# Optimization experiments

Hardware: AMD Instinct MI355X
Metric: run time of the kernel (lower is better)

The kernel has to match this reference:

```python
import jax, jax.numpy as jnp
import numpy as np

EPS = 1e-6
ALPHA = 0.2  # LeakyReLU negative slope


def layer_norm(x, g, b):
    mu = jnp.mean(x, axis=-1, keepdims=True)
    var = jnp.mean(jnp.square(x - mu), axis=-1, keepdims=True)
    return (x - mu) * jax.lax.rsqrt(var + EPS) * g + b


def graph_attention(x, bias, W, a_src, a_dst):
    # x: [B,N,D], bias: [B,N,N], W: [D, H*Dh], a_src/a_dst: [H, Dh]
    B, N, D = x.shape
    H, Dh = a_src.shape
    h = jnp.einsum('bnd,dhk->bhnk', x, W.reshape(D, H, Dh))  # [B,H,N,Dh]
    s = jnp.einsum('bhnk,hk->bhn', h, a_src)                 # source term
    t = jnp.einsum('bhnk,hk->bhn', h, a_dst)                 # target term
    e = jax.nn.leaky_relu(s[:, :, :, None] + t[:, :, None, :], ALPHA)
    e = e + bias[:, None, :, :]                              # graph mask/bias
    attn = jax.nn.softmax(e, axis=-1)                        # [B,H,N,N]
    out = jnp.einsum('bhij,bhjk->bhik', attn, h)             # [B,H,N,Dh]
    return out.transpose(0, 2, 1, 3).reshape(B, N, H * Dh)


def setup_inputs() -> dict:
    key = jax.random.key(0)
    ks = jax.random.split(key, 8)
    B, N, D, H = 2, 2048, 512, 8
    Dh = D // H
    sc = 1.0 / np.sqrt(D)
    return {
        'x': jax.random.normal(ks[0], (B, N, D), jnp.float32),
        'bias': jax.random.normal(ks[1], (B, N, N), jnp.float32),
        'W1': jax.random.normal(ks[2], (D, D), jnp.float32) * sc,
        'a_src1': jax.random.normal(ks[3], (H, Dh), jnp.float32) * sc,
        'a_dst1': jax.random.normal(ks[4], (H, Dh), jnp.float32) * sc,
        'g1': jnp.ones((D,), jnp.float32),
        'b1': jnp.zeros((D,), jnp.float32),
        'W2': jax.random.normal(ks[5], (D, D), jnp.float32) * sc,
        'a_src2': jax.random.normal(ks[6], (1, D), jnp.float32) * sc,
        'a_dst2': jax.random.normal(ks[7], (1, D), jnp.float32) * sc,
        'g2': jnp.ones((D,), jnp.float32),
        'b2': jnp.zeros((D,), jnp.float32),
    }


def reference(x, bias, W1, a_src1, a_dst1, g1, b1, W2, a_src2, a_dst2, g2, b2):
    # dropout is identity in eval mode
    attn_in = layer_norm(x, g1, b1)
    attn = graph_attention(attn_in, bias, W1, a_src1, a_dst1) + x
    attn_in2 = layer_norm(attn, g2, b2)
    out = graph_attention(attn_in2, bias, W2, a_src2, a_dst2) + attn
    return out
```

## Files before the change

kernel.cpp:

```cpp
#include <hip/hip_runtime.h>
#include <math.h>

#define NB 2
#define NN 2048
#define DD 512
#define L2E 1.44269504088896340736f

typedef __attribute__((ext_vector_type(8))) short short8;
typedef __attribute__((ext_vector_type(4))) float f32x4;

__device__ __forceinline__ unsigned short f2bf(float x) {
  union { float f; unsigned u; } a;
  a.f = x;
  unsigned r = a.u + 0x7FFF + ((a.u >> 16) & 1);
  return (unsigned short)(r >> 16);
}
__device__ __forceinline__ float bf2f(unsigned short u) {
  union { unsigned u; float f; } a;
  a.u = ((unsigned)u) << 16;
  return a.f;
}
__device__ __forceinline__ unsigned cvtpk(float lo, float hi) {
  unsigned r;
  asm("v_cvt_pk_bf16_f32 %0, %1, %2" : "=v"(r) : "v"(lo), "v"(hi));
  return r;
}
__device__ __forceinline__ uint2 exp4pk(float e0, float e1, float e2, float e3) {
  float p0, p1, p2, p3;
  uint2 d;
  asm("v_exp_f32 %2, %6\n\t"
      "v_exp_f32 %3, %7\n\t"
      "v_exp_f32 %4, %8\n\t"
      "v_exp_f32 %5, %9\n\t"
      "v_cvt_pk_bf16_f32 %0, %2, %3\n\t"
      "v_cvt_pk_bf16_f32 %1, %4, %5"
      : "=&v"(d.x), "=&v"(d.y), "=&v"(p0), "=&v"(p1), "=&v"(p2), "=&v"(p3)
      : "v"(e0), "v"(e1), "v"(e2), "v"(e3));
  return d;
}

__device__ __forceinline__ float waveReduceSum(float v) {
#pragma unroll
  for (int o = 32; o; o >>= 1) v += __shfl_down(v, o, 64);
  return v;
}
__device__ __forceinline__ float blockReduceSum(float v, float* red4) {
  int tid = threadIdx.x;
  __syncthreads();
  v = waveReduceSum(v);
  if ((tid & 63) == 0) red4[tid >> 6] = v;
  __syncthreads();
  return red4[0] + red4[1] + red4[2] + red4[3];
}

__global__ __launch_bounds__(256) void prep_kernel(
    const float* __restrict__ W1, const float* __restrict__ W2,
    unsigned short* __restrict__ WT1, unsigned short* __restrict__ WT2,
    const float* __restrict__ as1, const float* __restrict__ ad1,
    float* __restrict__ vs1, float* __restrict__ vd1,
    const float* __restrict__ as2, const float* __restrict__ ad2,
    float* __restrict__ vs2, float* __restrict__ vd2) {
  __shared__ float tile[64][65];
  int bid = blockIdx.x;
  int t = threadIdx.x;
  if (bid < 128) {
    const float* W = (bid & 64) ? W2 : W1;
    unsigned short* WT = (bid & 64) ? WT2 : WT1;
    int r = bid & 63;
    int kt = (r >> 3) * 64, ct = (r & 7) * 64;
#pragma unroll
    for (int u = 0; u < 16; u++) {
      int lin = t + u * 256;
      int kl = lin >> 6, cl = lin & 63;
      tile[kl][cl] = W[(size_t)(kt + kl) * DD + ct + cl];
    }
    __syncthreads();
#pragma unroll
    for (int u = 0; u < 16; u++) {
      int lin = t + u * 256;
      int cl = lin >> 6, kl = lin & 63;
      WT[(size_t)(ct + cl) * DD + kt + kl] = f2bf(tile[kl][cl]);
    }
  } else {
    int idx = bid - 128;
    int slot = idx >> 3, dch = idx & 7;
    const float *W, *as, *ad;
    float *vs, *vd;
    int Dh, hoff;
    if (slot < 8) {
      W = W1; as = as1 + slot * 64; ad = ad1 + slot * 64;
      vs = vs1 + (size_t)slot * DD; vd = vd1 + (size_t)slot * DD;
      Dh = 64; hoff = slot * 64;
    } else {
      W = W2; as = as2; ad = ad2; vs = vs2; vd = vd2;
      Dh = 512; hoff = 0;
    }
    int dl = t >> 2, kq = t & 3;
    int d = dch * 64 + dl;
    int kn = Dh >> 2;
    const float* wr = W + (size_t)d * DD + hoff + kq * kn;
    const float* asp = as + kq * kn;
    const float* adp = ad + kq * kn;
    float s = 0.f, dd2 = 0.f;
    for (int k = 0; k < kn; k++) {
      float wv = wr[k];
      s += wv * asp[k];
      dd2 += wv * adp[k];
    }
    s += __shfl_xor(s, 1);
    s += __shfl_xor(s, 2);
    dd2 += __shfl_xor(dd2, 1);
    dd2 += __shfl_xor(dd2, 2);
    if (kq == 0) {
      vs[d] = s;
      vd[d] = dd2;
    }
  }
}

__global__ __launch_bounds__(256) void lnst_kernel(
    const float* __restrict__ x, const float* __restrict__ g,
    const float* __restrict__ bb, unsigned short* __restrict__ y,
    const float* __restrict__ vs, const float* __restrict__ vd,
    float* __restrict__ sOut, float* __restrict__ tOut, int HN) {
  __shared__ float red4[4];
  __shared__ float lnS[512];
  int row = blockIdx.x;
  int t = threadIdx.x;
  const float* xr = x + (size_t)row * DD;
  float2 v = *(const float2*)&xr[2 * t];
  float s = blockReduceSum(v.x + v.y, red4);
  float mu = s * (1.0f / 512.0f);
  float d0 = v.x - mu, d1 = v.y - mu;
  float ss = blockReduceSum(d0 * d0 + d1 * d1, red4);
  float rstd = rsqrtf(ss * (1.0f / 512.0f) + 1e-6f);
  float2 gg = *(const float2*)&g[2 * t];
  float2 bv = *(const float2*)&bb[2 * t];
  float n0 = d0 * rstd * gg.x + bv.x;
  float n1 = d1 * rstd * gg.y + bv.y;
  ushort2 o;
  o.x = f2bf(n0);
  o.y = f2bf(n1);
  *(ushort2*)&y[(size_t)row * DD + 2 * t] = o;
  lnS[2 * t] = n0;
  lnS[2 * t + 1] = n1;
  __syncthreads();
  int wv = t >> 6, l = t & 63;
  int b = row >> 11, n = row & (NN - 1);
  float4 x0 = *(const float4*)&lnS[l * 8];
  float4 x1 = *(const float4*)&lnS[l * 8 + 4];
  for (int h = wv; h < HN; h += 4) {
    const float* vsr = vs + (size_t)h * DD + l * 8;
    const float* vdr = vd + (size_t)h * DD + l * 8;
    float4 a0 = *(const float4*)vsr, a1 = *(const float4*)(vsr + 4);
    float4 c0 = *(const float4*)vdr, c1 = *(const float4*)(vdr + 4);
    float ps = x0.x * a0.x + x0.y * a0.y + x0.z * a0.z + x0.w * a0.w +
               x1.x * a1.x + x1.y * a1.y + x1.z * a1.z + x1.w * a1.w;
    float pd = x0.x * c0.x + x0.y * c0.y + x0.z * c0.z + x0.w * c0.w +
               x1.x * c1.x + x1.y * c1.y + x1.z * c1.z + x1.w * c1.w;
#pragma unroll
    for (int o2 = 32; o2; o2 >>= 1) {
      ps += __shfl_xor(ps, o2);
      pd += __shfl_xor(pd, o2);
    }
    if (l == 0) {
      sOut[((size_t)b * HN + h) * NN + n] = ps * L2E;
      tOut[((size_t)b * HN + h) * NN + n] = pd * L2E;
    }
  }
}

__global__ __launch_bounds__(256) void gemm_kernel(const unsigned short* __restrict__ A,
                                                   const unsigned short* __restrict__ BT,
                                                   unsigned short* __restrict__ hbT) {
  __shared__ float accL[4][16][65];
  int t = threadIdx.x, w = t >> 6, l = t & 63;
  int li = l & 15, lg = l >> 4;
  int R0 = blockIdx.x * 16;
  int c0 = blockIdx.y * 64;
  const unsigned short* ar = A + (size_t)(R0 + li) * DD + w * 128 + lg * 8;
  const unsigned short* br = BT + (size_t)(c0 + li) * DD + w * 128 + lg * 8;
  f32x4 acc[4] = {};
#pragma unroll
  for (int k0 = 0; k0 < 128; k0 += 32) {
    short8 af = *(const short8*)(ar + k0);
#pragma unroll
    for (int f = 0; f < 4; f++) {
      short8 bf = *(const short8*)(br + (size_t)f * 16 * DD + k0);
      acc[f] = __builtin_amdgcn_mfma_f32_16x16x32_bf16(af, bf, acc[f], 0, 0, 0);
    }
  }
#pragma unroll
  for (int f = 0; f < 4; f++)
#pragma unroll
    for (int r = 0; r < 4; r++) accL[w][lg * 4 + r][f * 16 + li] = acc[f][r];
  __syncthreads();
  int b = R0 >> 11, jT = (R0 & (NN - 1)) >> 4;
#pragma unroll
  for (int u = 0; u < 2; u++) {
    int idx = t + u * 256;
    int f = idx >> 7;
    int rem = idx & 127;
    int cl = rem >> 3, jlp = rem & 7;
    int cc = f * 16 + cl;
    float v0 = accL[0][2 * jlp][cc] + accL[1][2 * jlp][cc] + accL[2][2 * jlp][cc] +
               accL[3][2 * jlp][cc];
    float v1 = accL[0][2 * jlp + 1][cc] + accL[1][2 * jlp + 1][cc] +
               accL[2][2 * jlp + 1][cc] + accL[3][2 * jlp + 1][cc];
    size_t off = (((size_t)(b * (DD / 64) + blockIdx.y) * (NN / 16)) + jT) * 1024 +
                 f * 256 + cl * 16 + jlp * 2;
    *(unsigned*)(hbT + off) = cvtpk(v0, v1);
  }
}

__global__ __launch_bounds__(256) void pvg_kernel(
    const unsigned short* __restrict__ hbT, const float* __restrict__ bias,
    const float* __restrict__ sArr, const float* __restrict__ tArr,
    const float* __restrict__ res, float* __restrict__ out) {
  __shared__ __align__(16) unsigned char smem[16896];
  unsigned short (*Pl)[2][1024] = (unsigned short (*)[2][1024])smem;
  float (*accL2)[16][65] = (float (*)[16][65])smem;
  float (*sLa)[16] = (float (*)[16])(smem + 8320);
  int t = threadIdx.x, w = t >> 6, l = t & 63;
  int jh = w & 1, hp = w >> 1;
  int li = l & 15, lg = l >> 4;
  int i0 = blockIdx.x * 16;
  int h0 = blockIdx.y * 2, b = blockIdx.z;
  int head = h0 + hp;
  size_t bhN = (size_t)(b * 8 + head) * NN;
  const float* trow = tArr + bhN;

  int rs = l >> 3, js = (l & 7) * 8, jc = l & 7;
  int wchunk = ((jc & 4) | ((jc & 3) ^ (rs & 3))) * 8;
  float sv[2];
  sv[0] = sArr[bhN + i0 + rs];
  sv[1] = sArr[bhN + i0 + 8 + rs];
  const float* bb0 = bias + ((size_t)b * NN + i0 + rs) * NN;
  const float* bb1 = bb0 + (size_t)8 * NN;

  const unsigned short* vbase =
      hbT + ((size_t)(b * 8 + head) * (NN / 16)) * 1024 + (lg >> 1) * 1024 + li * 16 +
      (lg & 1) * 8;
  int ra0 = li * 64 + (lg ^ (li & 3)) * 8;
  int ra1 = ra0 + 32;

  union { short8 v; unsigned short q[8]; } ones;
#pragma unroll
  for (int k = 0; k < 8; k++) ones.q[k] = 0x3F80;

  const int jbeg = jh * (NN / 2), jend = jbeg + NN / 2;
  f32x4 acc[4] = {};
  f32x4 accS = {0.f, 0.f, 0.f, 0.f};

  auto loadTB = [&](int j, float4& t0, float4& t1, float4& b0a, float4& b0b,
                    float4& b1a, float4& b1b) {
    t0 = *(const float4*)&trow[j + js];
    t1 = *(const float4*)&trow[j + js + 4];
    b0a = *(const float4*)&bb0[j + js];
    b0b = *(const float4*)&bb0[j + js + 4];
    b1a = *(const float4*)&bb1[j + js];
    b1b = *(const float4*)&bb1[j + js + 4];
  };
  auto computeP = [&](const float4& t0, const float4& t1, const float4& b0a,
                      const float4& b0b, const float4& b1a, const float4& b1b, int pb) {
#pragma unroll
    for (int u = 0; u < 2; u++) {
      const float4& ba = u ? b1a : b0a;
      const float4& bc = u ? b1b : b0b;
      int row = u * 8 + rs;
      float e0 = sv[u] + t0.x, e1 = sv[u] + t0.y;
      float e2 = sv[u] + t0.z, e3 = sv[u] + t0.w;
      float e4 = sv[u] + t1.x, e5 = sv[u] + t1.y;
      float e6 = sv[u] + t1.z, e7 = sv[u] + t1.w;
      e0 = fmaf(ba.x, L2E, fmaxf(e0, 0.2f * e0));
      e1 = fmaf(ba.y, L2E, fmaxf(e1, 0.2f * e1));
      e2 = fmaf(ba.z, L2E, fmaxf(e2, 0.2f * e2));
      e3 = fmaf(ba.w, L2E, fmaxf(e3, 0.2f * e3));
      e4 = fmaf(bc.x, L2E, fmaxf(e4, 0.2f * e4));
      e5 = fmaf(bc.y, L2E, fmaxf(e5, 0.2f * e5));
      e6 = fmaf(bc.z, L2E, fmaxf(e6, 0.2f * e6));
      e7 = fmaf(bc.w, L2E, fmaxf(e7, 0.2f * e7));
      uint2 d0 = exp4pk(e0, e1, e2, e3);
      uint2 d1 = exp4pk(e4, e5, e6, e7);
      uint4 dd;
      dd.x = d0.x; dd.y = d0.y; dd.z = d1.x; dd.w = d1.y;
      *(uint4*)&Pl[w][pb][row * 64 + wchunk] = dd;
    }
  };

  float4 tA0, tA1, bA0, bA1, bA2, bA3;

  loadTB(jbeg, tA0, tA1, bA0, bA1, bA2, bA3);
  computeP(tA0, tA1, bA0, bA1, bA2, bA3, 0);
  loadTB(jbeg + 64, tA0, tA1, bA0, bA1, bA2, bA3);

  int buf = 0;
  for (int jt = jbeg; jt < jend; jt += 64) {
    const unsigned short* vp = vbase + (size_t)jt * 64;
    short8 v0 = *(const short8*)(vp + 0);
    short8 v1 = *(const short8*)(vp + 256);
    short8 v2 = *(const short8*)(vp + 512);
    short8 v3 = *(const short8*)(vp + 768);
    short8 v4 = *(const short8*)(vp + 2048);
    short8 v5 = *(const short8*)(vp + 2304);
    short8 v6 = *(const short8*)(vp + 2560);
    short8 v7 = *(const short8*)(vp + 2816);
    short8 a0 = *(const short8*)&Pl[w][buf][ra0];
    short8 a1 = *(const short8*)&Pl[w][buf][ra1];
    if (jt + 64 < jend) {
      float4 n0 = tA0, n1 = tA1, m0 = bA0, m1 = bA1, m2 = bA2, m3 = bA3;
      int jn = (jt + 128 < jend) ? (jt + 128) : jbeg;
      loadTB(jn, tA0, tA1, bA0, bA1, bA2, bA3);
      computeP(n0, n1, m0, m1, m2, m3, buf ^ 1);
    }
    __builtin_amdgcn_s_setprio(1);
    accS = __builtin_amdgcn_mfma_f32_16x16x32_bf16(a0, ones.v, accS, 0, 0, 0);
    acc[0] = __builtin_amdgcn_mfma_f32_16x16x32_bf16(a0, v0, acc[0], 0, 0, 0);
    acc[1] = __builtin_amdgcn_mfma_f32_16x16x32_bf16(a0, v1, acc[1], 0, 0, 0);
    acc[2] = __builtin_amdgcn_mfma_f32_16x16x32_bf16(a0, v2, acc[2], 0, 0, 0);
    acc[3] = __builtin_amdgcn_mfma_f32_16x16x32_bf16(a0, v3, acc[3], 0, 0, 0);
    accS = __builtin_amdgcn_mfma_f32_16x16x32_bf16(a1, ones.v, accS, 0, 0, 0);
    acc[0] = __builtin_amdgcn_mfma_f32_16x16x32_bf16(a1, v4, acc[0], 0, 0, 0);
    acc[1] = __builtin_amdgcn_mfma_f32_16x16x32_bf16(a1, v5, acc[1], 0, 0, 0);
    acc[2] = __builtin_amdgcn_mfma_f32_16x16x32_bf16(a1, v6, acc[2], 0, 0, 0);
    acc[3] = __builtin_amdgcn_mfma_f32_16x16x32_bf16(a1, v7, acc[3], 0, 0, 0);
    __builtin_amdgcn_s_setprio(0);
    buf ^= 1;
  }

  __syncthreads();
  if (li == 0) {
#pragma unroll
    for (int r = 0; r < 4; r++) sLa[w][lg * 4 + r] = accS[r];
  }
#pragma unroll
  for (int hp2 = 0; hp2 < 2; hp2++) {
    if (hp == hp2) {
#pragma unroll
      for (int f = 0; f < 4; f++)
#pragma unroll
        for (int r = 0; r < 4; r++) accL2[jh][lg * 4 + r][f * 16 + li] = acc[f][r];
    }
    __syncthreads();
    {
      int rr = t >> 4, cq = t & 15;
      float S = sLa[2 * hp2][rr] + sLa[2 * hp2 + 1][rr];
      float inv = 1.0f / S;
      size_t ixb = ((size_t)b * NN + i0 + rr) * DD + (h0 + hp2) * 64 + cq;
#pragma unroll
      for (int f = 0; f < 4; f++) {
        int col = f * 16 + cq;
        float O = accL2[0][rr][col] + accL2[1][rr][col];
        out[ixb + f * 16] = O * inv + res[ixb + f * 16];
      }
    }
    __syncthreads();
  }
}

template <int HN, int CCH>
__global__ __launch_bounds__(256) void pv_kernel(
    const unsigned short* __restrict__ hbT, const float* __restrict__ bias,
    const float* __restrict__ sArr, const float* __restrict__ tArr,
    const float* __restrict__ res, float* __restrict__ out) {
  constexpr int DH = DD / HN;
  __shared__ __align__(16) unsigned char smem[16640];
  unsigned short (*Pl)[2][1024] = (unsigned short (*)[2][1024])smem;
  float (*accL)[16][33] = (float (*)[16][33])smem;
  float (*sLa)[16] = (float (*)[16])(smem + 8448);
  int t = threadIdx.x, w = t >> 6, l = t & 63;
  int li = l & 15, lg = l >> 4;
  int i0 = blockIdx.x * 16;
  int ck = blockIdx.y, bh = blockIdx.z;
  int h = bh % HN, b = bh / HN;
  int c0 = h * DH + ck * (CCH * 64);
  size_t bhN = (size_t)bh * NN;
  const float* trow = tArr + bhN;

  int rs = l >> 3, js = (l & 7) * 8, jc = l & 7;
  int wchunk = ((jc & 4) | ((jc & 3) ^ (rs & 3))) * 8;
  float sv[2];
  sv[0] = sArr[bhN + i0 + rs];
  sv[1] = sArr[bhN + i0 + 8 + rs];
  const float* bb0 = bias + ((size_t)b * NN + i0 + rs) * NN;
  const float* bb1 = bb0 + (size_t)8 * NN;

  const unsigned short* vbase =
      hbT + ((size_t)(b * (DD / 64) + (c0 >> 6)) * (NN / 16)) * 1024 +
      (lg >> 1) * 1024 + li * 16 + (lg & 1) * 8;
  int ra0 = li * 64 + (lg ^ (li & 3)) * 8;
  int ra1 = ra0 + 32;

  union { short8 v; unsigned short q[8]; } ones;
#pragma unroll
  for (int k = 0; k < 8; k++) ones.q[k] = 0x3F80;

  const int jbeg = w * (NN / 4), jend = jbeg + NN / 4;
  f32x4 acc[CCH][4] = {};
  f32x4 accS = {0.f, 0.f, 0.f, 0.f};

  auto loadTB = [&](int j, float4& t0, float4& t1, float4& b0a, float4& b0b,
                    float4& b1a, float4& b1b) {
    t0 = *(const float4*)&trow[j + js];
    t1 = *(const float4*)&trow[j + js + 4];
    b0a = *(const float4*)&bb0[j + js];
    b0b = *(const float4*)&bb0[j + js + 4];
    b1a = *(const float4*)&bb1[j + js];
    b1b = *(const float4*)&bb1[j + js + 4];
  };
  auto computeP = [&](const float4& t0, const float4& t1, const float4& b0a,
                      const float4& b0b, const float4& b1a, const float4& b1b, int pb) {
#pragma unroll
    for (int u = 0; u < 2; u++) {
      const float4& ba = u ? b1a : b0a;
      const float4& bc = u ? b1b : b0b;
      int row = u * 8 + rs;
      float e0 = sv[u] + t0.x, e1 = sv[u] + t0.y;
      float e2 = sv[u] + t0.z, e3 = sv[u] + t0.w;
      float e4 = sv[u] + t1.x, e5 = sv[u] + t1.y;
      float e6 = sv[u] + t1.z, e7 = sv[u] + t1.w;
      e0 = fmaf(ba.x, L2E, fmaxf(e0, 0.2f * e0));
      e1 = fmaf(ba.y, L2E, fmaxf(e1, 0.2f * e1));
      e2 = fmaf(ba.z, L2E, fmaxf(e2, 0.2f * e2));
      e3 = fmaf(ba.w, L2E, fmaxf(e3, 0.2f * e3));
      e4 = fmaf(bc.x, L2E, fmaxf(e4, 0.2f * e4));
      e5 = fmaf(bc.y, L2E, fmaxf(e5, 0.2f * e5));
      e6 = fmaf(bc.z, L2E, fmaxf(e6, 0.2f * e6));
      e7 = fmaf(bc.w, L2E, fmaxf(e7, 0.2f * e7));
      uint2 d0 = exp4pk(e0, e1, e2, e3);
      uint2 d1 = exp4pk(e4, e5, e6, e7);
      uint4 dd;
      dd.x = d0.x; dd.y = d0.y; dd.z = d1.x; dd.w = d1.y;
      *(uint4*)&Pl[w][pb][row * 64 + wchunk] = dd;
    }
  };
  auto loadV = [&](int jt, short8 (&vv)[CCH][8]) {
#pragma unroll
    for (int cc = 0; cc < CCH; cc++) {
      const unsigned short* vp =
          vbase + (size_t)cc * ((NN / 16) * 1024) + (size_t)jt * 64;
#pragma unroll
      for (int f = 0; f < 4; f++) {
        vv[cc][f] = *(const short8*)(vp + f * 256);
        vv[cc][4 + f] = *(const short8*)(vp + 2048 + f * 256);
      }
    }
  };
  auto domfma = [&](short8 a0, short8 a1, const short8 (&vv)[CCH][8]) {
    __builtin_amdgcn_s_setprio(1);
    accS = __builtin_amdgcn_mfma_f32_16x16x32_bf16(a0, ones.v, accS, 0, 0, 0);
#pragma unroll
    for (int cc = 0; cc < CCH; cc++)
#pragma unroll
      for (int f = 0; f < 4; f++)
        acc[cc][f] =
            __builtin_amdgcn_mfma_f32_16x16x32_bf16(a0, vv[cc][f], acc[cc][f], 0, 0, 0);
    accS = __builtin_amdgcn_mfma_f32_16x16x32_bf16(a1, ones.v, accS, 0, 0, 0);
#pragma unroll
    for (int cc = 0; cc < CCH; cc++)
#pragma unroll
      for (int f = 0; f < 4; f++)
        acc[cc][f] =
            __builtin_amdgcn_mfma_f32_16x16x32_bf16(a1, vv[cc][4 + f], acc[cc][f], 0, 0, 0);
    __builtin_amdgcn_s_setprio(0);
  };

  float4 tA0, tA1, bA0, bA1, bA2, bA3;
  short8 vv[CCH][8];

  loadTB(jbeg, tA0, tA1, bA0, bA1, bA2, bA3);
  computeP(tA0, tA1, bA0, bA1, bA2, bA3, 0);
  loadTB(jbeg + 64, tA0, tA1, bA0, bA1, bA2, bA3);

  int buf = 0;
  for (int jt = jbeg; jt < jend; jt += 64) {
    loadV(jt, vv);
    short8 a0 = *(const short8*)&Pl[w][buf][ra0];
    short8 a1 = *(const short8*)&Pl[w][buf][ra1];
    if (jt + 64 < jend) {
      float4 n0 = tA0, n1 = tA1, m0 = bA0, m1 = bA1, m2 = bA2, m3 = bA3;
      int jn = (jt + 128 < jend) ? (jt + 128) : jbeg;
      loadTB(jn, tA0, tA1, bA0, bA1, bA2, bA3);
      computeP(n0, n1, m0, m1, m2, m3, buf ^ 1);
    }
    domfma(a0, a1, vv);
    buf ^= 1;
  }

  __syncthreads();
  if (li == 0) {
#pragma unroll
    for (int r = 0; r < 4; r++) sLa[w][lg * 4 + r] = accS[r];
  }
#pragma unroll
  for (int g = 0; g < 2 * CCH; g++) {
    int cc = g >> 1, half = g & 1;
#pragma unroll
    for (int f = 0; f < 2; f++)
#pragma unroll
      for (int r = 0; r < 4; r++)
        accL[w][lg * 4 + r][f * 16 + li] = acc[cc][half * 2 + f][r];
    __syncthreads();
    {
      int rr = t >> 4, cp = (t & 15) * 2;
      float S = sLa[0][rr] + sLa[1][rr] + sLa[2][rr] + sLa[3][rr];
      float inv = 1.0f / S;
      float2 O = {0.f, 0.f};
#pragma unroll
      for (int w2 = 0; w2 < 4; w2++) {
        O.x += accL[w2][rr][cp];
        O.y += accL[w2][rr][cp + 1];
      }
      size_t ix = ((size_t)b * NN + i0 + rr) * DD + c0 + cc * 64 + half * 32 + cp;
      float2 rv = *(const float2*)&res[ix];
      float2 ov = {O.x * inv + rv.x, O.y * inv + rv.y};
      *(float2*)&out[ix] = ov;
    }
    __syncthreads();
  }
}

extern "C" void kernel_launch(void* const* d_in, const int* in_sizes, int n_in,
                              void* d_out, int out_size, void* d_ws, size_t ws_size,
                              hipStream_t stream) {
  const float* x = (const float*)d_in[0];
  const float* bias = (const float*)d_in[1];
  const float* W1 = (const float*)d_in[2];
  const float* asrc1 = (const float*)d_in[3];
  const float* adst1 = (const float*)d_in[4];
  const float* g1 = (const float*)d_in[5];
  const float* b1 = (const float*)d_in[6];
  const float* W2 = (const float*)d_in[7];
  const float* asrc2 = (const float*)d_in[8];
  const float* adst2 = (const float*)d_in[9];
  const float* g2 = (const float*)d_in[10];
  const float* b2 = (const float*)d_in[11];
  float* out = (float*)d_out;
  float* ws = (float*)d_ws;

  const size_t RC = (size_t)NB * NN * DD;
  float* attnBuf = ws;
  unsigned short* lnB = (unsigned short*)(ws + RC);
  unsigned short* hbT = (unsigned short*)(ws + RC + RC / 2);
  unsigned short* WT1 = (unsigned short*)(ws + 2 * RC);
  unsigned short* WT2 = WT1 + (size_t)DD * DD;
  float* vs1 = (float*)(WT2 + (size_t)DD * DD);
  float* vd1 = vs1 + 8 * DD;
  float* vs2 = vd1 + 8 * DD;
  float* vd2 = vs2 + DD;
  float* sBuf = vd2 + DD;
  float* tBuf = sBuf + 16 * NN;

  const int rows = NB * NN;

  hipLaunchKernelGGL(prep_kernel, dim3(128 + 72), dim3(256), 0, stream, W1, W2, WT1, WT2,
                     asrc1, adst1, vs1, vd1, asrc2, adst2, vs2, vd2);

  hipLaunchKernelGGL(lnst_kernel, dim3(rows), dim3(256), 0, stream, x, g1, b1, lnB, vs1, vd1,
                     sBuf, tBuf, 8);
  hipLaunchKernelGGL(gemm_kernel, dim3(256, 8), dim3(256), 0, stream, lnB, WT1, hbT);
  hipLaunchKernelGGL(pvg_kernel, dim3(128, 4, 2), dim3(256), 0, stream, hbT, bias, sBuf,
                     tBuf, x, attnBuf);

  hipLaunchKernelGGL(lnst_kernel, dim3(rows), dim3(256), 0, stream, attnBuf, g2, b2, lnB, vs2,
                     vd2, sBuf, tBuf, 1);
  hipLaunchKernelGGL(gemm_kernel, dim3(256, 8), dim3(256), 0, stream, lnB, WT2, hbT);
  hipLaunchKernelGGL((pv_kernel<1, 2>), dim3(128, 4, 2), dim3(256), 0, stream, hbT, bias,
                     sBuf, tBuf, attnBuf, out);
}
```

Baseline: 152.2 us.

## Build P fragments directly in registers in pvg_kernel, dropping LDS staging

In pvg_kernel each lane now computes the exp(leaky_relu+bias) values for its own MFMA A-operand layout (row ri, column group jq) and packs them straight into short8 fragments. This removes the shared-memory round trip for P, the double buffer and the swizzled reads, and cuts LDS use to 8.5KB. Bias is prefetched one tile ahead, but the t loads now happen inside each iteration. The bias access pattern also changes to 16 rows per wave with 8-float pieces, which may coalesce less well.

```diff
diff --git a/kernel.cpp b/kernel.cpp
--- a/kernel.cpp
+++ b/kernel.cpp
@@ -217,17 +217,143 @@
     const unsigned short* __restrict__ hbT, const float* __restrict__ bias,
     const float* __restrict__ sArr, const float* __restrict__ tArr,
     const float* __restrict__ res, float* __restrict__ out) {
-  __shared__ __align__(16) unsigned char smem[16896];
-  unsigned short (*Pl)[2][1024] = (unsigned short (*)[2][1024])smem;
+  __shared__ __align__(16) unsigned char smem[8576];
   float (*accL2)[16][65] = (float (*)[16][65])smem;
   float (*sLa)[16] = (float (*)[16])(smem + 8320);
   int t = threadIdx.x, w = t >> 6, l = t & 63;
   int jh = w & 1, hp = w >> 1;
-  int li = l & 15, lg = l >> 4;
+  int ri = l & 15, jq = l >> 4;
   int i0 = blockIdx.x * 16;
   int h0 = blockIdx.y * 2, b = blockIdx.z;
   int head = h0 + hp;
   size_t bhN = (size_t)(b * 8 + head) * NN;
+  const float* trow = tArr + bhN;
+
+  float sv = sArr[bhN + i0 + ri];
+  const float* bbr = bias + ((size_t)b * NN + i0 + ri) * NN;
+
+  const unsigned short* vbase =
+      hbT + ((size_t)(b * 8 + head) * (NN / 16)) * 1024 + (jq >> 1) * 1024 + ri * 16 +
+      (jq & 1) * 8;
+
+  union { short8 v; unsigned short q[8]; } ones;
+#pragma unroll
+  for (int k = 0; k < 8; k++) ones.q[k] = 0x3F80;
+
+  const int jbeg = jh * (NN / 2), jend = jbeg + NN / 2;
+  f32x4 acc[4] = {};
+  f32x4 accS = {0.f, 0.f, 0.f, 0.f};
+
+  int jo = jq * 8;
+
+  auto loadB = [&](int j, float4& q0, float4& q1, float4& q2, float4& q3) {
+    q0 = *(const float4*)&bbr[j + jo];
+    q1 = *(const float4*)&bbr[j + jo + 4];
+    q2 = *(const float4*)&bbr[j + 32 + jo];
+    q3 = *(const float4*)&bbr[j + 32 + jo + 4];
+  };
+  auto mkfrag = [&](const float4& t0, const float4& t1, const float4& b0,
+                    const float4& b1) -> short8 {
+    float e0 = sv + t0.x, e1 = sv + t0.y, e2 = sv + t0.z, e3 = sv + t0.w;
+    float e4 = sv + t1.x, e5 = sv + t1.y, e6 = sv + t1.z, e7 = sv + t1.w;
+    e0 = fmaf(b0.x, L2E, fmaxf(e0, 0.2f * e0));
+    e1 = fmaf(b0.y, L2E, fmaxf(e1, 0.2f * e1));
+    e2 = fmaf(b0.z, L2E, fmaxf(e2, 0.2f * e2));
+    e3 = fmaf(b0.w, L2E, fmaxf(e3, 0.2f * e3));
+    e4 = fmaf(b1.x, L2E, fmaxf(e4, 0.2f * e4));
+    e5 = fmaf(b1.y, L2E, fmaxf(e5, 0.2f * e5));
+    e6 = fmaf(b1.z, L2E, fmaxf(e6, 0.2f * e6));
+    e7 = fmaf(b1.w, L2E, fmaxf(e7, 0.2f * e7));
+    union { short8 v; uint2 u[2]; } r;
+    r.u[0] = exp4pk(e0, e1, e2, e3);
+    r.u[1] = exp4pk(e4, e5, e6, e7);
+    return r.v;
+  };
+
+  float4 cb0, cb1, cb2, cb3;
+  loadB(jbeg, cb0, cb1, cb2, cb3);
+
+  for (int jt = jbeg; jt < jend; jt += 64) {
+    const unsigned short* vp = vbase + (size_t)jt * 64;
+    short8 v0 = *(const short8*)(vp + 0);
+    short8 v1 = *(const short8*)(vp + 256);
+    short8 v2 = *(const short8*)(vp + 512);
+    short8 v3 = *(const short8*)(vp + 768);
+    short8 v4 = *(const short8*)(vp + 2048);
+    short8 v5 = *(const short8*)(vp + 2304);
+    short8 v6 = *(const short8*)(vp + 2560);
+    short8 v7 = *(const short8*)(vp + 2816);
+    float4 t0 = *(const float4*)&trow[jt + jo];
+    float4 t1 = *(const float4*)&trow[jt + jo + 4];
+    float4 t2 = *(const float4*)&trow[jt + 32 + jo];
+    float4 t3 = *(const float4*)&trow[jt + 32 + jo + 4];
+    float4 nb0, nb1, nb2, nb3;
+    int jn = (jt + 64 < jend) ? (jt + 64) : jbeg;
+    loadB(jn, nb0, nb1, nb2, nb3);
+    short8 a0 = mkfrag(t0, t1, cb0, cb1);
+    short8 a1 = mkfrag(t2, t3, cb2, cb3);
+    __builtin_amdgcn_s_setprio(1);
+    accS = __builtin_amdgcn_mfma_f32_16x16x32_bf16(a0, ones.v, accS, 0, 0, 0);
+    acc[0] = __builtin_amdgcn_mfma_f32_16x16x32_bf16(a0, v0, acc[0], 0, 0, 0);
+    acc[1] = __builtin_amdgcn_mfma_f32_16x16x32_bf16(a0, v1, acc[1], 0, 0, 0);
+    acc[2] = __builtin_amdgcn_mfma_f32_16x16x32_bf16(a0, v2, acc[2], 0, 0, 0);
+    acc[3] = __builtin_amdgcn_mfma_f32_16x16x32_bf16(a0, v3, acc[3], 0, 0, 0);
+    accS = __builtin_amdgcn_mfma_f32_16x16x32_bf16(a1, ones.v, accS, 0, 0, 0);
+    acc[0] = __builtin_amdgcn_mfma_f32_16x16x32_bf16(a1, v4, acc[0], 0, 0, 0);
+    acc[1] = __builtin_amdgcn_mfma_f32_16x16x32_bf16(a1, v5, acc[1], 0, 0, 0);
+    acc[2] = __builtin_amdgcn_mfma_f32_16x16x32_bf16(a1, v6, acc[2], 0, 0, 0);
+    acc[3] = __builtin_amdgcn_mfma_f32_16x16x32_bf16(a1, v7, acc[3], 0, 0, 0);
+    __builtin_amdgcn_s_setprio(0);
+    cb0 = nb0; cb1 = nb1; cb2 = nb2; cb3 = nb3;
+  }
+
+  __syncthreads();
+  if (ri == 0) {
+#pragma unroll
+    for (int r = 0; r < 4; r++) sLa[w][jq * 4 + r] = accS[r];
+  }
+#pragma unroll
+  for (int hp2 = 0; hp2 < 2; hp2++) {
+    if (hp == hp2) {
+#pragma unroll
+      for (int f = 0; f < 4; f++)
+#pragma unroll
+        for (int r = 0; r < 4; r++) accL2[jh][jq * 4 + r][f * 16 + ri] = acc[f][r];
+    }
+    __syncthreads();
+    {
+      int rr = t >> 4, cq = t & 15;
+      float S = sLa[2 * hp2][rr] + sLa[2 * hp2 + 1][rr];
+      float inv = 1.0f / S;
+      size_t ixb = ((size_t)b * NN + i0 + rr) * DD + (h0 + hp2) * 64 + cq;
+#pragma unroll
+      for (int f = 0; f < 4; f++) {
+        int col = f * 16 + cq;
+        float O = accL2[0][rr][col] + accL2[1][rr][col];
+        out[ixb + f * 16] = O * inv + res[ixb + f * 16];
+      }
+    }
+    __syncthreads();
+  }
+}
+
+template <int HN, int CCH>
+__global__ __launch_bounds__(256) void pv_kernel(
+    const unsigned short* __restrict__ hbT, const float* __restrict__ bias,
+    const float* __restrict__ sArr, const float* __restrict__ tArr,
+    const float* __restrict__ res, float* __restrict__ out) {
+  constexpr int DH = DD / HN;
+  __shared__ __align__(16) unsigned char smem[16640];
+  unsigned short (*Pl)[2][1024] = (unsigned short (*)[2][1024])smem;
+  float (*accL)[16][33] = (float (*)[16][33])smem;
+  float (*sLa)[16] = (float (*)[16])(smem + 8448);
+  int t = threadIdx.x, w = t >> 6, l = t & 63;
+  int li = l & 15, lg = l >> 4;
+  int i0 = blockIdx.x * 16;
+  int ck = blockIdx.y, bh = blockIdx.z;
+  int h = bh % HN, b = bh / HN;
+  int c0 = h * DH + ck * (CCH * 64);
+  size_t bhN = (size_t)bh * NN;
   const float* trow = tArr + bhN;
 
   int rs = l >> 3, js = (l & 7) * 8, jc = l & 7;
@@ -239,8 +365,8 @@
   const float* bb1 = bb0 + (size_t)8 * NN;
 
   const unsigned short* vbase =
-      hbT + ((size_t)(b * 8 + head) * (NN / 16)) * 1024 + (lg >> 1) * 1024 + li * 16 +
-      (lg & 1) * 8;
+      hbT + ((size_t)(b * (DD / 64) + (c0 >> 6)) * (NN / 16)) * 1024 +
+      (lg >> 1) * 1024 + li * 16 + (lg & 1) * 8;
   int ra0 = li * 64 + (lg ^ (li & 3)) * 8;
   int ra1 = ra0 + 32;
 
@@ -248,8 +374,8 @@
 #pragma unroll
   for (int k = 0; k < 8; k++) ones.q[k] = 0x3F80;
 
-  const int jbeg = jh * (NN / 2), jend = jbeg + NN / 2;
-  f32x4 acc[4] = {};
+  const int jbeg = w * (NN / 4), jend = jbeg + NN / 4;
+  f32x4 acc[CCH][4] = {};
   f32x4 accS = {0.f, 0.f, 0.f, 0.f};
 
   auto loadTB = [&](int j, float4& t0, float4& t1, float4& b0a, float4& b0b,
@@ -287,153 +413,6 @@
       *(uint4*)&Pl[w][pb][row * 64 + wchunk] = dd;
     }
   };
-
-  float4 tA0, tA1, bA0, bA1, bA2, bA3;
-
-  loadTB(jbeg, tA0, tA1, bA0, bA1, bA2, bA3);
-  computeP(tA0, tA1, bA0, bA1, bA2, bA3, 0);
-  loadTB(jbeg + 64, tA0, tA1, bA0, bA1, bA2, bA3);
-
-  int buf = 0;
-  for (int jt = jbeg; jt < jend; jt += 64) {
-    const unsigned short* vp = vbase + (size_t)jt * 64;
-    short8 v0 = *(const short8*)(vp + 0);
-    short8 v1 = *(const short8*)(vp + 256);
-    short8 v2 = *(const short8*)(vp + 512);
-    short8 v3 = *(const short8*)(vp + 768);
-    short8 v4 = *(const short8*)(vp + 2048);
-    short8 v5 = *(const short8*)(vp + 2304);
-    short8 v6 = *(const short8*)(vp + 2560);
-    short8 v7 = *(const short8*)(vp + 2816);
-    short8 a0 = *(const short8*)&Pl[w][buf][ra0];
-    short8 a1 = *(const short8*)&Pl[w][buf][ra1];
-    if (jt + 64 < jend) {
-      float4 n0 = tA0, n1 = tA1, m0 = bA0, m1 = bA1, m2 = bA2, m3 = bA3;
-      int jn = (jt + 128 < jend) ? (jt + 128) : jbeg;
-      loadTB(jn, tA0, tA1, bA0, bA1, bA2, bA3);
-      computeP(n0, n1, m0, m1, m2, m3, buf ^ 1);
-    }
-    __builtin_amdgcn_s_setprio(1);
-    accS = __builtin_amdgcn_mfma_f32_16x16x32_bf16(a0, ones.v, accS, 0, 0, 0);
-    acc[0] = __builtin_amdgcn_mfma_f32_16x16x32_bf16(a0, v0, acc[0], 0, 0, 0);
-    acc[1] = __builtin_amdgcn_mfma_f32_16x16x32_bf16(a0, v1, acc[1], 0, 0, 0);
-    acc[2] = __builtin_amdgcn_mfma_f32_16x16x32_bf16(a0, v2, acc[2], 0, 0, 0);
-    acc[3] = __builtin_amdgcn_mfma_f32_16x16x32_bf16(a0, v3, acc[3], 0, 0, 0);
-    accS = __builtin_amdgcn_mfma_f32_16x16x32_bf16(a1, ones.v, accS, 0, 0, 0);
-    acc[0] = __builtin_amdgcn_mfma_f32_16x16x32_bf16(a1, v4, acc[0], 0, 0, 0);
-    acc[1] = __builtin_amdgcn_mfma_f32_16x16x32_bf16(a1, v5, acc[1], 0, 0, 0);
-    acc[2] = __builtin_amdgcn_mfma_f32_16x16x32_bf16(a1, v6, acc[2], 0, 0, 0);
-    acc[3] = __builtin_amdgcn_mfma_f32_16x16x32_bf16(a1, v7, acc[3], 0, 0, 0);
-    __builtin_amdgcn_s_setprio(0);
-    buf ^= 1;
-  }
-
-  __syncthreads();
-  if (li == 0) {
-#pragma unroll
-    for (int r = 0; r < 4; r++) sLa[w][lg * 4 + r] = accS[r];
-  }
-#pragma unroll
-  for (int hp2 = 0; hp2 < 2; hp2++) {
-    if (hp == hp2) {
-#pragma unroll
-      for (int f = 0; f < 4; f++)
-#pragma unroll
-        for (int r = 0; r < 4; r++) accL2[jh][lg * 4 + r][f * 16 + li] = acc[f][r];
-    }
-    __syncthreads();
-    {
-      int rr = t >> 4, cq = t & 15;
-      float S = sLa[2 * hp2][rr] + sLa[2 * hp2 + 1][rr];
-      float inv = 1.0f / S;
-      size_t ixb = ((size_t)b * NN + i0 + rr) * DD + (h0 + hp2) * 64 + cq;
-#pragma unroll
-      for (int f = 0; f < 4; f++) {
-        int col = f * 16 + cq;
-        float O = accL2[0][rr][col] + accL2[1][rr][col];
-        out[ixb + f * 16] = O * inv + res[ixb + f * 16];
-      }
-    }
-    __syncthreads();
-  }
-}
-
-template <int HN, int CCH>
-__global__ __launch_bounds__(256) void pv_kernel(
-    const unsigned short* __restrict__ hbT, const float* __restrict__ bias,
-    const float* __restrict__ sArr, const float* __restrict__ tArr,
-    const float* __restrict__ res, float* __restrict__ out) {
-  constexpr int DH = DD / HN;
-  __shared__ __align__(16) unsigned char smem[16640];
-  unsigned short (*Pl)[2][1024] = (unsigned short (*)[2][1024])smem;
-  float (*accL)[16][33] = (float (*)[16][33])smem;
-  float (*sLa)[16] = (float (*)[16])(smem + 8448);
-  int t = threadIdx.x, w = t >> 6, l = t & 63;
-  int li = l & 15, lg = l >> 4;
-  int i0 = blockIdx.x * 16;
-  int ck = blockIdx.y, bh = blockIdx.z;
-  int h = bh % HN, b = bh / HN;
-  int c0 = h * DH + ck * (CCH * 64);
-  size_t bhN = (size_t)bh * NN;
-  const float* trow = tArr + bhN;
-
-  int rs = l >> 3, js = (l & 7) * 8, jc = l & 7;
-  int wchunk = ((jc & 4) | ((jc & 3) ^ (rs & 3))) * 8;
-  float sv[2];
-  sv[0] = sArr[bhN + i0 + rs];
-  sv[1] = sArr[bhN + i0 + 8 + rs];
-  const float* bb0 = bias + ((size_t)b * NN + i0 + rs) * NN;
-  const float* bb1 = bb0 + (size_t)8 * NN;
-
-  const unsigned short* vbase =
-      hbT + ((size_t)(b * (DD / 64) + (c0 >> 6)) * (NN / 16)) * 1024 +
-      (lg >> 1) * 1024 + li * 16 + (lg & 1) * 8;
-  int ra0 = li * 64 + (lg ^ (li & 3)) * 8;
-  int ra1 = ra0 + 32;
-
-  union { short8 v; unsigned short q[8]; } ones;
-#pragma unroll
-  for (int k = 0; k < 8; k++) ones.q[k] = 0x3F80;
-
-  const int jbeg = w * (NN / 4), jend = jbeg + NN / 4;
-  f32x4 acc[CCH][4] = {};
-  f32x4 accS = {0.f, 0.f, 0.f, 0.f};
-
-  auto loadTB = [&](int j, float4& t0, float4& t1, float4& b0a, float4& b0b,
-                    float4& b1a, float4& b1b) {
-    t0 = *(const float4*)&trow[j + js];
-    t1 = *(const float4*)&trow[j + js + 4];
-    b0a = *(const float4*)&bb0[j + js];
-    b0b = *(const float4*)&bb0[j + js + 4];
-    b1a = *(const float4*)&bb1[j + js];
-    b1b = *(const float4*)&bb1[j + js + 4];
-  };
-  auto computeP = [&](const float4& t0, const float4& t1, const float4& b0a,
-                      const float4& b0b, const float4& b1a, const float4& b1b, int pb) {
-#pragma unroll
-    for (int u = 0; u < 2; u++) {
-      const float4& ba = u ? b1a : b0a;
-      const float4& bc = u ? b1b : b0b;
-      int row = u * 8 + rs;
-      float e0 = sv[u] + t0.x, e1 = sv[u] + t0.y;
-      float e2 = sv[u] + t0.z, e3 = sv[u] + t0.w;
-      float e4 = sv[u] + t1.x, e5 = sv[u] + t1.y;
-      float e6 = sv[u] + t1.z, e7 = sv[u] + t1.w;
-      e0 = fmaf(ba.x, L2E, fmaxf(e0, 0.2f * e0));
-      e1 = fmaf(ba.y, L2E, fmaxf(e1, 0.2f * e1));
-      e2 = fmaf(ba.z, L2E, fmaxf(e2, 0.2f * e2));
-      e3 = fmaf(ba.w, L2E, fmaxf(e3, 0.2f * e3));
-      e4 = fmaf(bc.x, L2E, fmaxf(e4, 0.2f * e4));
-      e5 = fmaf(bc.y, L2E, fmaxf(e5, 0.2f * e5));
-      e6 = fmaf(bc.z, L2E, fmaxf(e6, 0.2f * e6));
-      e7 = fmaf(bc.w, L2E, fmaxf(e7, 0.2f * e7));
-      uint2 d0 = exp4pk(e0, e1, e2, e3);
-      uint2 d1 = exp4pk(e4, e5, e6, e7);
-      uint4 dd;
-      dd.x = d0.x; dd.y = d0.y; dd.z = d1.x; dd.w = d1.y;
-      *(uint4*)&Pl[w][pb][row * 64 + wchunk] = dd;
-    }
-  };
   auto loadV = [&](int jt, short8 (&vv)[CCH][8]) {
 #pragma unroll
     for (int cc = 0; cc < CCH; cc++) {
```

Result: slower. 171.9 us (+13.0%).
